# Optimization experiments

Measured on AMD Instinct MI355X. Metric: run time of the kernel, lower is better.

The kernel has to match this reference:

```python
import jax, jax.numpy as jnp
import numpy as np

N_NODES = 100000
N_EDGES = 200000
N_ATOM_FEATS = 56
HIDDEN = 256
N_GRAPHS = 2048
OUT_DIM = 1
EPS = 1e-5  # torch BatchNorm1d default


def setup_inputs() -> dict:
    key = jax.random.key(0)
    ks = jax.random.split(key, 10)
    x = jax.random.randint(ks[0], (N_NODES, N_ATOM_FEATS), 0, 2, dtype=jnp.int64 if jax.config.jax_enable_x64 else jnp.int32)
    edge_index = jax.random.randint(ks[1], (2, N_EDGES), 0, N_NODES)
    batch = jnp.sort(jax.random.randint(ks[2], (N_NODES,), 0, N_GRAPHS))
    emb_tables = jax.random.normal(ks[3], (N_ATOM_FEATS, 2, HIDDEN), dtype=jnp.float32) * 0.1
    Ws = jax.random.normal(ks[4], (3, HIDDEN, HIDDEN), dtype=jnp.float32) * (1.0 / np.sqrt(HIDDEN))
    bs = jnp.zeros((3, HIDDEN), dtype=jnp.float32)
    gammas = jnp.ones((2, HIDDEN), dtype=jnp.float32)
    betas = jnp.zeros((2, HIDDEN), dtype=jnp.float32)
    lin_w = jax.random.normal(ks[5], (HIDDEN, OUT_DIM), dtype=jnp.float32) * (1.0 / np.sqrt(HIDDEN))
    lin_b = jnp.zeros((OUT_DIM,), dtype=jnp.float32)
    return {"x": x, "edge_index": edge_index, "batch": batch, "emb_tables": emb_tables,
            "Ws": Ws, "bs": bs, "gammas": gammas, "betas": betas, "lin_w": lin_w, "lin_b": lin_b}


def reference(x, edge_index, batch, emb_tables, Ws, bs, gammas, betas, lin_w, lin_b):
    n = x.shape[0]
    # --- AtomEncoder: sum of 56 per-feature embedding lookups ---
    # emb_tables: [56, 2, H]; x: [N, 56] -> gathered [N, 56, H] -> sum over feature axis
    feat_idx = jnp.arange(x.shape[1])[None, :]  # [1,56]
    h = emb_tables[feat_idx, x].sum(axis=1)      # [N, H]

    # --- GCN normalization with self-loops (shared across layers) ---
    loops = jnp.arange(n)
    src = jnp.concatenate([edge_index[0], loops])
    dst = jnp.concatenate([edge_index[1], loops])
    deg = jax.ops.segment_sum(jnp.ones_like(src, dtype=h.dtype), dst, num_segments=n)
    dinv = jnp.where(deg > 0, jax.lax.rsqrt(deg), 0.0)
    norm = dinv[src] * dinv[dst]  # [E+N]

    def gcn_conv(h, W, b):
        hw = h @ W                                   # [N, H']
        msg = hw[src] * norm[:, None]                # gather + scale
        agg = jax.ops.segment_sum(msg, dst, num_segments=n)  # scatter-add
        return agg + b

    # --- layers 0..L-2: conv -> batchnorm (batch stats) -> relu; eval => no dropout ---
    for i in range(2):
        h = gcn_conv(h, Ws[i], bs[i])
        mu = h.mean(axis=0)
        var = h.var(axis=0)
        h = (h - mu) * jax.lax.rsqrt(var + EPS) * gammas[i] + betas[i]
        h = jax.nn.relu(h)
    # --- last conv (return_embeds=True: no softmax) ---
    h = gcn_conv(h, Ws[2], bs[2])

    # --- global mean pool over graphs ---
    sums = jax.ops.segment_sum(h, batch, num_segments=N_GRAPHS)          # [G, H]
    counts = jax.ops.segment_sum(jnp.ones((n,), h.dtype), batch, num_segments=N_GRAPHS)
    pooled = sums / jnp.maximum(counts, 1.0)[:, None]

    return pooled @ lin_w + lin_b  # [G, OUT_DIM]
```

## Files before the change

### kernel.cpp

```cpp
#include <hip/hip_runtime.h>
#include <hip/hip_bf16.h>

#define NN 100000
#define NE 200000
#define NF 56
#define HD 256
#define NG 2048

#define SCAN_CH 512
#define NCH ((NN + SCAN_CH - 1) / SCAN_CH)
#define EB ((NE + 255) / 256)

#define PB 2048
#define AB 2048
#define ZB 98

typedef __bf16 bf16x8 __attribute__((ext_vector_type(8)));
typedef __bf16 bf16x4 __attribute__((ext_vector_type(4)));
typedef float  floatx4 __attribute__((ext_vector_type(4)));

__global__ void prep_params(const float* __restrict__ emb, const float* __restrict__ Ws,
                            const float* __restrict__ bs, const float* __restrict__ lw,
                            __bf16* __restrict__ dW0t, float* __restrict__ bW0,
                            float* __restrict__ w2lw, float* __restrict__ b2lw,
                            __bf16* __restrict__ Wt, unsigned* __restrict__ deg) {
    __shared__ float row[HD];
    int c = threadIdx.x;
    int f = blockIdx.x;
    if (f >= NF + 2) {
        int g = f - (NF + 2);
        if (g < HD) {
            Wt[(size_t)g * HD + c] = (__bf16)Ws[(size_t)HD * HD + (size_t)c * HD + g];
        } else {
            int idx = (g - HD) * HD + c;
            if (idx < NN / 4) ((int4*)deg)[idx] = make_int4(0, 0, 0, 0);
        }
        return;
    }
    if (f == NF + 1) {
        const float* W2 = Ws + (size_t)2 * HD * HD;
        float acc = 0.f;
        for (int k = 0; k < HD; ++k) acc += W2[(size_t)c * HD + k] * lw[k];
        w2lw[c] = acc;
        row[c] = bs[2 * HD + c] * lw[c];
        __syncthreads();
        for (int off = 128; off > 0; off >>= 1) {
            if (c < off) row[c] += row[c + off];
            __syncthreads();
        }
        if (c == 0) *b2lw = row[0];
        return;
    }
    if (f < NF) {
        row[c] = emb[(f * 2 + 1) * HD + c] - emb[(f * 2 + 0) * HD + c];
    } else {
        float s = 0.f;
        for (int ff = 0; ff < NF; ++ff) s += emb[(ff * 2) * HD + c];
        row[c] = s;
    }
    __syncthreads();
    float acc = 0.f;
    for (int k = 0; k < HD; ++k) acc += row[k] * Ws[k * HD + c];
    if (f < NF) {
        dW0t[c * 64 + f] = (__bf16)acc;
    } else {
        bW0[c] = acc;
        #pragma unroll
        for (int k = NF; k < 64; ++k) dW0t[c * 64 + k] = (__bf16)0.f;
    }
}

__global__ void deg_kernel(const int* __restrict__ dst, unsigned* __restrict__ deg, int E) {
    int e = blockIdx.x * blockDim.x + threadIdx.x;
    if (e < E) atomicAdd(&deg[dst[e]], 1u);
}

__global__ void chunk_sum_dinv(const unsigned* __restrict__ deg, unsigned* __restrict__ csum,
                               float* __restrict__ dinv, float* __restrict__ selfn) {
    __shared__ unsigned s[SCAN_CH];
    int t = threadIdx.x;
    int base = blockIdx.x * SCAN_CH;
    unsigned v = (base + t < NN) ? deg[base + t] : 0u;
    s[t] = v;
    if (base + t < NN) {
        float d = (float)(v + 1u);
        dinv[base + t]  = rsqrtf(d);
        selfn[base + t] = 1.0f / d;
    }
    __syncthreads();
    for (int off = SCAN_CH / 2; off > 0; off >>= 1) {
        if (t < off) s[t] += s[t + off];
        __syncthreads();
    }
    if (t == 0) csum[blockIdx.x] = s[0];
}

__global__ void chunk_apply(const unsigned* __restrict__ deg, const unsigned* __restrict__ csum,
                            unsigned* __restrict__ row_start, unsigned* __restrict__ cursor) {
    __shared__ unsigned s[SCAN_CH];
    __shared__ unsigned cs[256];
    int t = threadIdx.x;
    if (t < 256) cs[t] = (t < NCH) ? csum[t] : 0u;
    __syncthreads();
    for (int off = 1; off < 256; off <<= 1) {
        unsigned add = (t < 256 && t >= off) ? cs[t - off] : 0u;
        __syncthreads();
        if (t < 256) cs[t] += add;
        __syncthreads();
    }
    unsigned chunk_base = (blockIdx.x == 0) ? 0u : cs[blockIdx.x - 1];

    int base = blockIdx.x * SCAN_CH;
    unsigned v = (base + t < NN) ? deg[base + t] : 0u;
    s[t] = v;
    __syncthreads();
    for (int off = 1; off < SCAN_CH; off <<= 1) {
        unsigned add = (t >= off) ? s[t - off] : 0u;
        __syncthreads();
        s[t] += add;
        __syncthreads();
    }
    if (base + t < NN) {
        unsigned rs = chunk_base + s[t] - v;
        row_start[base + t] = rs;
        cursor[base + t] = rs;
    }
    if (blockIdx.x == 0 && t == 0) row_start[NN] = NE;
}

__global__ void csr_fill_gb(const int* __restrict__ src, const int* __restrict__ dst,
                            const float* __restrict__ dinv, unsigned* __restrict__ cursor,
                            int* __restrict__ ecol, float* __restrict__ enorm,
                            const int* __restrict__ batch, unsigned* __restrict__ gstart) {
    int t = threadIdx.x;
    if (blockIdx.x < EB) {
        int e = blockIdx.x * 256 + t;
        if (e < NE) {
            int s = src[e], d = dst[e];
            unsigned pos = atomicAdd(&cursor[d], 1u);
            ecol[pos] = s;
            enorm[pos] = dinv[s] * dinv[d];
        }
    } else {
        int g = (blockIdx.x - EB) * 256 + t;
        if (g <= NG) {
            int lo = 0, hi = NN;
            while (lo < hi) {
                int mid = (lo + hi) >> 1;
                if (batch[mid] < g) lo = mid + 1; else hi = mid;
            }
            gstart[g] = (unsigned)lo;
        }
    }
}

#define ELSTR 68
__global__ void __launch_bounds__(512) encoder_mfma(const int* __restrict__ x,
                                                    const __bf16* __restrict__ dW0t,
                                                    const float* __restrict__ bW0,
                                                    __bf16* __restrict__ C) {
    __shared__ __bf16 sA[128 * ELSTR];
    __shared__ __bf16 sB[256 * ELSTR];
    int t = threadIdx.x;
    int m0 = blockIdx.x * 128;
    int lane = t & 63, w = t >> 6;
    int quad = lane >> 4, l16 = lane & 15;
    int mw = (w & 1) * 64, nw = (w >> 1) * 64;

    {
        int r = t >> 2;
        int kh = (t & 3) * 16;
        int row = m0 + r;
        int nreal = (kh < 48) ? 16 : 8;
        #pragma unroll
        for (int j = 0; j < 4; ++j) {
            bf16x4 b;
            if (row < NN && j * 4 < nreal) {
                int4 iv = *(const int4*)&x[(size_t)row * NF + kh + j * 4];
                b[0] = (__bf16)(float)iv.x;
                b[1] = (__bf16)(float)iv.y;
                b[2] = (__bf16)(float)iv.z;
                b[3] = (__bf16)(float)iv.w;
            } else {
                b[0] = b[1] = b[2] = b[3] = (__bf16)0.f;
            }
            *(bf16x4*)&sA[r * ELSTR + kh + j * 4] = b;
        }
    }
    {
        int bn = t >> 1;
        int kh = (t & 1) * 32;
        #pragma unroll
        for (int j = 0; j < 4; ++j) {
            bf16x8 v = *(const bf16x8*)&dW0t[(size_t)bn * 64 + kh + j * 8];
            *(bf16x8*)&sB[bn * ELSTR + kh + j * 8] = v;
        }
    }
    __syncthreads();

    floatx4 acc[4][4] = {};
    #pragma unroll
    for (int s = 0; s < 2; ++s) {
        bf16x8 af[4], bfr[4];
        #pragma unroll
        for (int i = 0; i < 4; ++i)
            af[i] = *(const bf16x8*)&sA[(mw + i * 16 + l16) * ELSTR + s * 32 + quad * 8];
        #pragma unroll
        for (int i = 0; i < 4; ++i)
            bfr[i] = *(const bf16x8*)&sB[(nw + i * 16 + l16) * ELSTR + s * 32 + quad * 8];
        #pragma unroll
        for (int mi = 0; mi < 4; ++mi)
            #pragma unroll
            for (int ni = 0; ni < 4; ++ni)
                acc[mi][ni] = __builtin_amdgcn_mfma_f32_16x16x32_bf16(
                    af[mi], bfr[ni], acc[mi][ni], 0, 0, 0);
    }

    float bw[4];
    #pragma unroll
    for (int ni = 0; ni < 4; ++ni) bw[ni] = bW0[nw + ni * 16 + l16];
    #pragma unroll
    for (int mi = 0; mi < 4; ++mi) {
        #pragma unroll
        for (int r = 0; r < 4; ++r) {
            int row = m0 + mw + mi * 16 + quad * 4 + r;
            if (row < NN) {
                #pragma unroll
                for (int ni = 0; ni < 4; ++ni)
                    C[(size_t)row * HD + nw + ni * 16 + l16] =
                        (__bf16)(acc[mi][ni][r] + bw[ni]);
            }
        }
    }
}

#define LSTR 36
__global__ void __launch_bounds__(512) gemm_mfma(const __bf16* __restrict__ A,
                                                 const __bf16* __restrict__ Wt,
                                                 __bf16* __restrict__ C, int M,
                                                 const float* __restrict__ ascale,
                                                 const float* __restrict__ ashift) {
    __shared__ __bf16 sA[128 * LSTR];
    __shared__ __bf16 sB[256 * LSTR];
    int t = threadIdx.x;
    int m0 = blockIdx.x * 128;
    int lane = t & 63, w = t >> 6;
    int quad = lane >> 4, l16 = lane & 15;
    int mw = (w & 1) * 64;
    int nw = (w >> 1) * 64;

    int ar = t >> 2;
    int ak = (t & 3) * 8;
    int bn = t >> 1;
    int bk = (t & 1) * 16;

    auto ldA = [&](int k0, bf16x8& pa) {
        float4 s0 = *(const float4*)&ascale[k0 + ak];
        float4 s1 = *(const float4*)&ascale[k0 + ak + 4];
        float4 h0 = *(const float4*)&ashift[k0 + ak];
        float4 h1 = *(const float4*)&ashift[k0 + ak + 4];
        int row = m0 + ar;
        bf16x8 a = {};
        if (row < M) a = *(const bf16x8*)&A[(size_t)row * HD + k0 + ak];
        bf16x8 b;
        b[0] = (__bf16)fmaxf((float)a[0] * s0.x + h0.x, 0.f);
        b[1] = (__bf16)fmaxf((float)a[1] * s0.y + h0.y, 0.f);
        b[2] = (__bf16)fmaxf((float)a[2] * s0.z + h0.z, 0.f);
        b[3] = (__bf16)fmaxf((float)a[3] * s0.w + h0.w, 0.f);
        b[4] = (__bf16)fmaxf((float)a[4] * s1.x + h1.x, 0.f);
        b[5] = (__bf16)fmaxf((float)a[5] * s1.y + h1.y, 0.f);
        b[6] = (__bf16)fmaxf((float)a[6] * s1.z + h1.z, 0.f);
        b[7] = (__bf16)fmaxf((float)a[7] * s1.w + h1.w, 0.f);
        pa = b;
    };
    auto ldB = [&](int k0, bf16x8 pb[2]) {
        #pragma unroll
        for (int j = 0; j < 2; ++j)
            pb[j] = *(const bf16x8*)&Wt[(size_t)bn * HD + k0 + bk + j * 8];
    };

    bf16x8 pa, pb[2];
    ldA(0, pa);
    ldB(0, pb);

    floatx4 acc[4][4] = {};

    for (int k0 = 0; k0 < 256; k0 += 32) {
        *(bf16x8*)&sA[ar * LSTR + ak] = pa;
        *(bf16x8*)&sB[bn * LSTR + bk]     = pb[0];
        *(bf16x8*)&sB[bn * LSTR + bk + 8] = pb[1];
        __syncthreads();

        if (k0 + 32 < 256) {
            ldA(k0 + 32, pa);
            ldB(k0 + 32, pb);
        }

        bf16x8 af[4], bfr[4];
        #pragma unroll
        for (int i = 0; i < 4; ++i)
            af[i] = *(const bf16x8*)&sA[(mw + i * 16 + l16) * LSTR + quad * 8];
        #pragma unroll
        for (int i = 0; i < 4; ++i)
            bfr[i] = *(const bf16x8*)&sB[(nw + i * 16 + l16) * LSTR + quad * 8];
        #pragma unroll
        for (int mi = 0; mi < 4; ++mi)
            #pragma unroll
            for (int ni = 0; ni < 4; ++ni)
                acc[mi][ni] = __builtin_amdgcn_mfma_f32_16x16x32_bf16(
                    af[mi], bfr[ni], acc[mi][ni], 0, 0, 0);
        __syncthreads();
    }

    #pragma unroll
    for (int mi = 0; mi < 4; ++mi) {
        #pragma unroll
        for (int r = 0; r < 4; ++r) {
            int row = m0 + mw + mi * 16 + quad * 4 + r;
            if (row < M) {
                #pragma unroll
                for (int ni = 0; ni < 4; ++ni)
                    C[(size_t)row * HD + nw + ni * 16 + l16] = (__bf16)acc[mi][ni][r];
            }
        }
    }
}

__global__ void __launch_bounds__(256) gcn_aggregate(const __bf16* __restrict__ hw,
                                                     const float* __restrict__ selfn,
                                                     const float* __restrict__ bias,
                                                     const unsigned* __restrict__ row_start,
                                                     const int* __restrict__ ecol,
                                                     const float* __restrict__ enorm,
                                                     __bf16* __restrict__ agg,
                                                     float* __restrict__ part) {
    int t = threadIdx.x;
    int l = t & 63, w = t >> 6;
    int c4 = l * 4;
    float4 bv = *(const float4*)&bias[c4];
    float4 lsum = make_float4(0.f, 0.f, 0.f, 0.f);
    float4 lssq = make_float4(0.f, 0.f, 0.f, 0.f);

    for (int n = blockIdx.x * 4 + w; n < NN; n += AB * 4) {
        float s = selfn[n];
        bf16x4 hv = *(const bf16x4*)&hw[(size_t)n * HD + c4];
        float4 acc;
        acc.x = (float)hv[0] * s + bv.x;
        acc.y = (float)hv[1] * s + bv.y;
        acc.z = (float)hv[2] * s + bv.z;
        acc.w = (float)hv[3] * s + bv.w;
        unsigned e0 = row_start[n], e1 = row_start[n + 1];
        unsigned e = e0;
        for (; e + 4 <= e1; e += 4) {
            int sv0 = ecol[e], sv1 = ecol[e + 1], sv2 = ecol[e + 2], sv3 = ecol[e + 3];
            float nm0 = enorm[e], nm1 = enorm[e + 1], nm2 = enorm[e + 2], nm3 = enorm[e + 3];
            bf16x4 u0 = *(const bf16x4*)&hw[(size_t)sv0 * HD + c4];
            bf16x4 u1 = *(const bf16x4*)&hw[(size_t)sv1 * HD + c4];
            bf16x4 u2 = *(const bf16x4*)&hw[(size_t)sv2 * HD + c4];
            bf16x4 u3 = *(const bf16x4*)&hw[(size_t)sv3 * HD + c4];
            acc.x += (float)u0[0] * nm0 + (float)u1[0] * nm1 + (float)u2[0] * nm2 + (float)u3[0] * nm3;
            acc.y += (float)u0[1] * nm0 + (float)u1[1] * nm1 + (float)u2[1] * nm2 + (float)u3[1] * nm3;
            acc.z += (float)u0[2] * nm0 + (float)u1[2] * nm1 + (float)u2[2] * nm2 + (float)u3[2] * nm3;
            acc.w += (float)u0[3] * nm0 + (float)u1[3] * nm1 + (float)u2[3] * nm2 + (float)u3[3] * nm3;
        }
        for (; e + 2 <= e1; e += 2) {
            int sv0 = ecol[e], sv1 = ecol[e + 1];
            float nm0 = enorm[e], nm1 = enorm[e + 1];
            bf16x4 u0 = *(const bf16x4*)&hw[(size_t)sv0 * HD + c4];
            bf16x4 u1 = *(const bf16x4*)&hw[(size_t)sv1 * HD + c4];
            acc.x += (float)u0[0] * nm0 + (float)u1[0] * nm1;
            acc.y += (float)u0[1] * nm0 + (float)u1[1] * nm1;
            acc.z += (float)u0[2] * nm0 + (float)u1[2] * nm1;
            acc.w += (float)u0[3] * nm0 + (float)u1[3] * nm1;
        }
        if (e < e1) {
            int sv = ecol[e];
            float nm = enorm[e];
            bf16x4 u = *(const bf16x4*)&hw[(size_t)sv * HD + c4];
            acc.x += (float)u[0] * nm;
            acc.y += (float)u[1] * nm;
            acc.z += (float)u[2] * nm;
            acc.w += (float)u[3] * nm;
        }
        bf16x4 o;
        o[0] = (__bf16)acc.x; o[1] = (__bf16)acc.y;
        o[2] = (__bf16)acc.z; o[3] = (__bf16)acc.w;
        *(bf16x4*)&agg[(size_t)n * HD + c4] = o;

        lsum.x += acc.x; lsum.y += acc.y; lsum.z += acc.z; lsum.w += acc.w;
        lssq.x += acc.x * acc.x; lssq.y += acc.y * acc.y;
        lssq.z += acc.z * acc.z; lssq.w += acc.w * acc.w;
    }

    __shared__ float4 ssum[4][64];
    __shared__ float4 sss[4][64];
    ssum[w][l] = lsum;
    sss[w][l]  = lssq;
    __syncthreads();
    if (w == 0) {
        float4 a0 = ssum[0][l], a1 = ssum[1][l], a2 = ssum[2][l], a3 = ssum[3][l];
        float4 q0 = sss[0][l],  q1 = sss[1][l],  q2 = sss[2][l],  q3 = sss[3][l];
        part[(c4 + 0) * AB + blockIdx.x] = a0.x + a1.x + a2.x + a3.x;
        part[(c4 + 1) * AB + blockIdx.x] = a0.y + a1.y + a2.y + a3.y;
        part[(c4 + 2) * AB + blockIdx.x] = a0.z + a1.z + a2.z + a3.z;
        part[(c4 + 3) * AB + blockIdx.x] = a0.w + a1.w + a2.w + a3.w;
        part[(HD + c4 + 0) * AB + blockIdx.x] = q0.x + q1.x + q2.x + q3.x;
        part[(HD + c4 + 1) * AB + blockIdx.x] = q0.y + q1.y + q2.y + q3.y;
        part[(HD + c4 + 2) * AB + blockIdx.x] = q0.z + q1.z + q2.z + q3.z;
        part[(HD + c4 + 3) * AB + blockIdx.x] = q0.w + q1.w + q2.w + q3.w;
    }
}

__global__ void __launch_bounds__(256) bn_scale(const float* __restrict__ part,
                                                const float* __restrict__ gamma,
                                                const float* __restrict__ beta,
                                                float* __restrict__ scale,
                                                float* __restrict__ shift) {
    __shared__ float rs[256], rq[256];
    int t = threadIdx.x;
    int c = blockIdx.x;
    float s = 0.f, q = 0.f;
    for (int j = t; j < PB; j += 256) {
        s += part[c * PB + j];
        q += part[(HD + c) * PB + j];
    }
    rs[t] = s; rq[t] = q;
    __syncthreads();
    for (int off = 128; off > 0; off >>= 1) {
        if (t < off) { rs[t] += rs[t + off]; rq[t] += rq[t + off]; }
        __syncthreads();
    }
    if (t == 0) {
        const float inv_n = 1.0f / (float)NN;
        float mu  = rs[0] * inv_n;
        float var = rq[0] * inv_n - mu * mu;
        float rstd = rsqrtf(var + 1e-5f);
        float sc = gamma[c] * rstd;
        scale[c] = sc;
        shift[c] = beta[c] - mu * sc;
    }
}

__global__ void __launch_bounds__(256) bn_dot(const __bf16* __restrict__ h,
                                              const float* __restrict__ scale,
                                              const float* __restrict__ shift,
                                              const float* __restrict__ w2lw,
                                              float* __restrict__ z) {
    int tid = blockIdx.x * 256 + threadIdx.x;
    int n = tid >> 6;
    if (n >= NN) return;
    int l = tid & 63;
    int c4 = l * 4;
    bf16x4 a = *(const bf16x4*)&h[(size_t)n * HD + c4];
    float4 sc = *(const float4*)&scale[c4];
    float4 sh = *(const float4*)&shift[c4];
    float4 wv = *(const float4*)&w2lw[c4];
    float d = fmaxf((float)a[0] * sc.x + sh.x, 0.f) * wv.x
            + fmaxf((float)a[1] * sc.y + sh.y, 0.f) * wv.y
            + fmaxf((float)a[2] * sc.z + sh.z, 0.f) * wv.z
            + fmaxf((float)a[3] * sc.w + sh.w, 0.f) * wv.w;
    #pragma unroll
    for (int off = 32; off > 0; off >>= 1) d += __shfl_down(d, off, 64);
    if (l == 0) z[n] = d;
}

__global__ void __launch_bounds__(256) pool_fused(const float* __restrict__ z,
                                                  const float* __restrict__ selfn,
                                                  const float* __restrict__ b2lw,
                                                  const unsigned* __restrict__ row_start,
                                                  const int* __restrict__ ecol,
                                                  const float* __restrict__ enorm,
                                                  const unsigned* __restrict__ gstart,
                                                  const float* __restrict__ lb,
                                                  float* __restrict__ out) {
    int tid = blockIdx.x * 256 + threadIdx.x;
    int g = tid >> 6;
    if (g >= NG) return;
    int l = tid & 63;
    unsigned s0 = gstart[g], s1 = gstart[g + 1];
    float bb = *b2lw;
    float s = 0.f;
    for (unsigned i = s0 + l; i < s1; i += 64) {
        float d = selfn[i] * z[i] + bb;
        unsigned e0 = row_start[i], e1 = row_start[i + 1];
        for (unsigned e = e0; e < e1; ++e)
            d += enorm[e] * z[ecol[e]];
        s += d;
    }
    #pragma unroll
    for (int off = 32; off > 0; off >>= 1) s += __shfl_down(s, off, 64);
    if (l == 0) out[g] = s / fmaxf((float)(s1 - s0), 1.0f) + lb[0];
}

extern "C" void kernel_launch(void* const* d_in, const int* in_sizes, int n_in,
                              void* d_out, int out_size, void* d_ws, size_t ws_size,
                              hipStream_t stream) {
    const int*   x     = (const int*)d_in[0];
    const int*   ei    = (const int*)d_in[1];
    const int*   batch = (const int*)d_in[2];
    const float* emb   = (const float*)d_in[3];
    const float* Ws    = (const float*)d_in[4];
    const float* bs    = (const float*)d_in[5];
    const float* gam   = (const float*)d_in[6];
    const float* bet   = (const float*)d_in[7];
    const float* lw    = (const float*)d_in[8];
    const float* lb    = (const float*)d_in[9];
    float* out = (float*)d_out;

    const int* src = ei;
    const int* dst = ei + NE;

    char* p = (char*)d_ws;
    size_t off = 0;
    auto carve = [&](size_t bytes) { void* r = p + off; off = (off + bytes + 255) & ~(size_t)255; return r; };
    __bf16*   buf0   = (__bf16*)carve((size_t)NN * HD * 2);
    __bf16*   buf1   = (__bf16*)carve((size_t)NN * HD * 2);
    float*    bW0    = (float*)carve(HD * 4);
    __bf16*   dW0t   = (__bf16*)carve(HD * 64 * 2);
    __bf16*   Wt     = (__bf16*)carve((size_t)HD * HD * 2);
    float*    w2lw   = (float*)carve(HD * 4);
    float*    b2lw   = (float*)carve(256);
    unsigned* deg    = (unsigned*)carve(NN * 4);
    float*    dinv   = (float*)carve(NN * 4);
    float*    selfn  = (float*)carve(NN * 4);
    unsigned* csum   = (unsigned*)carve(256 * 4);
    unsigned* row_s  = (unsigned*)carve((NN + 1) * 4);
    unsigned* cursor = (unsigned*)carve(NN * 4);
    int*      ecol   = (int*)carve(NE * 4);
    float*    enorm  = (float*)carve(NE * 4);
    float*    part   = (float*)carve((size_t)2 * HD * PB * 4);
    float*    scale  = (float*)carve(HD * 4);
    float*    shift  = (float*)carve(HD * 4);
    unsigned* gstart = (unsigned*)carve((NG + 1) * 4);
    float*    zbuf   = (float*)carve(NN * 4);
    (void)ws_size; (void)n_in; (void)in_sizes; (void)out_size;

    prep_params<<<NF + 2 + HD + ZB, HD, 0, stream>>>(
        emb, Ws, bs, lw, dW0t, bW0, w2lw, b2lw, Wt, deg);

    deg_kernel<<<(NE + 255) / 256, 256, 0, stream>>>(dst, deg, NE);
    chunk_sum_dinv<<<NCH, SCAN_CH, 0, stream>>>(deg, csum, dinv, selfn);
    chunk_apply<<<NCH, SCAN_CH, 0, stream>>>(deg, csum, row_s, cursor);
    csr_fill_gb<<<EB + (NG + 256) / 256, 256, 0, stream>>>(
        src, dst, dinv, cursor, ecol, enorm, batch, gstart);

    encoder_mfma<<<(NN + 127) / 128, 512, 0, stream>>>(x, dW0t, bW0, buf1);
    gcn_aggregate<<<AB, 256, 0, stream>>>(
        buf1, selfn, bs, row_s, ecol, enorm, buf0, part);
    bn_scale<<<HD, 256, 0, stream>>>(part, gam, bet, scale, shift);

    gemm_mfma<<<(NN + 127) / 128, 512, 0, stream>>>(
        buf0, Wt, buf1, NN, scale, shift);
    gcn_aggregate<<<AB, 256, 0, stream>>>(
        buf1, selfn, bs + HD, row_s, ecol, enorm, buf0, part);
    bn_scale<<<HD, 256, 0, stream>>>(part, gam + HD, bet + HD, scale, shift);

    bn_dot<<<(NN * 64 + 255) / 256, 256, 0, stream>>>(buf0, scale, shift, w2lw, zbuf);
    pool_fused<<<(NG * 64 + 255) / 256, 256, 0, stream>>>(
        zbuf, selfn, b2lw, row_s, ecol, enorm, gstart, lb, out);
}
```

Baseline: 290.1 us.

## Aggregate 64-wide encoder inputs before first GEMM instead of 256-wide features

Uses linearity of the first GCN layer: the binary atom features (plus a constant-1 column carrying the embedding base term) are aggregated over the graph in a 64-wide bf16 space, then multiplied by the folded embedding-times-W0 matrix. This replaces the first 256-wide gather/scatter aggregation pass with a much narrower one. The encoder GEMM now also emits the BatchNorm partial sums, and the partial-sum layout becomes row-major per block so bn_scale takes a variable block count. Extra costs are an x-to-bf16 conversion pass and bf16 rounding of the aggregated inputs before the GEMM.

New measurement: 274.1 us. 5.5% less time.

```diff
diff --git a/kernel.cpp b/kernel.cpp
--- a/kernel.cpp
+++ b/kernel.cpp
@@ -11,9 +11,10 @@
 #define NCH ((NN + SCAN_CH - 1) / SCAN_CH)
 #define EB ((NE + 255) / 256)
 
-#define PB 2048
 #define AB 2048
 #define ZB 98
+#define CVB ((NN + 255) / 256)
+#define ENB ((NN + 127) / 128)
 
 typedef __bf16 bf16x8 __attribute__((ext_vector_type(8)));
 typedef __bf16 bf16x4 __attribute__((ext_vector_type(4)));
@@ -21,9 +22,10 @@
 
 __global__ void prep_params(const float* __restrict__ emb, const float* __restrict__ Ws,
                             const float* __restrict__ bs, const float* __restrict__ lw,
-                            __bf16* __restrict__ dW0t, float* __restrict__ bW0,
+                            __bf16* __restrict__ dW0t,
                             float* __restrict__ w2lw, float* __restrict__ b2lw,
-                            __bf16* __restrict__ Wt, unsigned* __restrict__ deg) {
+                            __bf16* __restrict__ Wt, unsigned* __restrict__ deg,
+                            const int* __restrict__ x, __bf16* __restrict__ xb) {
     __shared__ float row[HD];
     int c = threadIdx.x;
     int f = blockIdx.x;
@@ -31,9 +33,29 @@
         int g = f - (NF + 2);
         if (g < HD) {
             Wt[(size_t)g * HD + c] = (__bf16)Ws[(size_t)HD * HD + (size_t)c * HD + g];
-        } else {
+        } else if (g < HD + ZB) {
             int idx = (g - HD) * HD + c;
             if (idx < NN / 4) ((int4*)deg)[idx] = make_int4(0, 0, 0, 0);
+        } else {
+            int r = (g - HD - ZB) * 256 + c;
+            if (r < NN) {
+                const int* xr = x + (size_t)r * NF;
+                __bf16 o[64];
+                #pragma unroll
+                for (int j = 0; j < 14; ++j) {
+                    int4 iv = *(const int4*)&xr[j * 4];
+                    o[j * 4 + 0] = (__bf16)(float)iv.x;
+                    o[j * 4 + 1] = (__bf16)(float)iv.y;
+                    o[j * 4 + 2] = (__bf16)(float)iv.z;
+                    o[j * 4 + 3] = (__bf16)(float)iv.w;
+                }
+                o[56] = (__bf16)1.0f;
+                #pragma unroll
+                for (int j = 57; j < 64; ++j) o[j] = (__bf16)0.0f;
+                #pragma unroll
+                for (int j = 0; j < 8; ++j)
+                    *(bf16x8*)&xb[(size_t)r * 64 + j * 8] = *(const bf16x8*)&o[j * 8];
+            }
         }
         return;
     }
@@ -64,9 +86,9 @@
     if (f < NF) {
         dW0t[c * 64 + f] = (__bf16)acc;
     } else {
-        bW0[c] = acc;
-        #pragma unroll
-        for (int k = NF; k < 64; ++k) dW0t[c * 64 + k] = (__bf16)0.f;
+        dW0t[c * 64 + 56] = (__bf16)acc;
+        #pragma unroll
+        for (int k = 57; k < 64; ++k) dW0t[c * 64 + k] = (__bf16)0.f;
     }
 }
 
@@ -154,13 +176,41 @@
     }
 }
 
+__global__ void __launch_bounds__(256) agg_x(const __bf16* __restrict__ xb,
+                                             const float* __restrict__ selfn,
+                                             const unsigned* __restrict__ row_start,
+                                             const int* __restrict__ ecol,
+                                             const float* __restrict__ enorm,
+                                             __bf16* __restrict__ ax) {
+    int tid = blockIdx.x * 256 + threadIdx.x;
+    int n = tid >> 6;
+    if (n >= NN) return;
+    int l = tid & 63;
+    float acc = (float)xb[(size_t)n * 64 + l] * selfn[n];
+    unsigned e0 = row_start[n], e1 = row_start[n + 1];
+    unsigned e = e0;
+    for (; e + 2 <= e1; e += 2) {
+        int s0 = ecol[e], s1 = ecol[e + 1];
+        float n0 = enorm[e], n1 = enorm[e + 1];
+        float v0 = (float)xb[(size_t)s0 * 64 + l];
+        float v1 = (float)xb[(size_t)s1 * 64 + l];
+        acc += v0 * n0 + v1 * n1;
+    }
+    if (e < e1)
+        acc += (float)xb[(size_t)ecol[e] * 64 + l] * enorm[e];
+    ax[(size_t)n * 64 + l] = (__bf16)acc;
+}
+
 #define ELSTR 68
-__global__ void __launch_bounds__(512) encoder_mfma(const int* __restrict__ x,
-                                                    const __bf16* __restrict__ dW0t,
-                                                    const float* __restrict__ bW0,
-                                                    __bf16* __restrict__ C) {
+__global__ void __launch_bounds__(512) enc_gemm(const __bf16* __restrict__ ax,
+                                                const __bf16* __restrict__ dW0t,
+                                                const float* __restrict__ b0,
+                                                __bf16* __restrict__ C,
+                                                float* __restrict__ part) {
     __shared__ __bf16 sA[128 * ELSTR];
     __shared__ __bf16 sB[256 * ELSTR];
+    __shared__ float psum[8][64];
+    __shared__ float psq[8][64];
     int t = threadIdx.x;
     int m0 = blockIdx.x * 128;
     int lane = t & 63, w = t >> 6;
@@ -169,32 +219,23 @@
 
     {
         int r = t >> 2;
-        int kh = (t & 3) * 16;
+        int k = (t & 3) * 16;
         int row = m0 + r;
-        int nreal = (kh < 48) ? 16 : 8;
-        #pragma unroll
-        for (int j = 0; j < 4; ++j) {
-            bf16x4 b;
-            if (row < NN && j * 4 < nreal) {
-                int4 iv = *(const int4*)&x[(size_t)row * NF + kh + j * 4];
-                b[0] = (__bf16)(float)iv.x;
-                b[1] = (__bf16)(float)iv.y;
-                b[2] = (__bf16)(float)iv.z;
-                b[3] = (__bf16)(float)iv.w;
-            } else {
-                b[0] = b[1] = b[2] = b[3] = (__bf16)0.f;
-            }
-            *(bf16x4*)&sA[r * ELSTR + kh + j * 4] = b;
-        }
+        bf16x8 v0 = {}, v1 = {};
+        if (row < NN) {
+            v0 = *(const bf16x8*)&ax[(size_t)row * 64 + k];
+            v1 = *(const bf16x8*)&ax[(size_t)row * 64 + k + 8];
+        }
+        *(bf16x8*)&sA[r * ELSTR + k]     = v0;
+        *(bf16x8*)&sA[r * ELSTR + k + 8] = v1;
     }
     {
         int bn = t >> 1;
         int kh = (t & 1) * 32;
         #pragma unroll
-        for (int j = 0; j < 4; ++j) {
-            bf16x8 v = *(const bf16x8*)&dW0t[(size_t)bn * 64 + kh + j * 8];
-            *(bf16x8*)&sB[bn * ELSTR + kh + j * 8] = v;
-        }
+        for (int j = 0; j < 4; ++j)
+            *(bf16x8*)&sB[bn * ELSTR + kh + j * 8] =
+                *(const bf16x8*)&dW0t[(size_t)bn * 64 + kh + j * 8];
     }
     __syncthreads();
 
@@ -218,7 +259,9 @@
 
     float bw[4];
     #pragma unroll
-    for (int ni = 0; ni < 4; ++ni) bw[ni] = bW0[nw + ni * 16 + l16];
+    for (int ni = 0; ni < 4; ++ni) bw[ni] = b0[nw + ni * 16 + l16];
+    float ls[4] = {0.f, 0.f, 0.f, 0.f};
+    float lq[4] = {0.f, 0.f, 0.f, 0.f};
     #pragma unroll
     for (int mi = 0; mi < 4; ++mi) {
         #pragma unroll
@@ -226,10 +269,36 @@
             int row = m0 + mw + mi * 16 + quad * 4 + r;
             if (row < NN) {
                 #pragma unroll
-                for (int ni = 0; ni < 4; ++ni)
-                    C[(size_t)row * HD + nw + ni * 16 + l16] =
-                        (__bf16)(acc[mi][ni][r] + bw[ni]);
+                for (int ni = 0; ni < 4; ++ni) {
+                    float v = acc[mi][ni][r] + bw[ni];
+                    C[(size_t)row * HD + nw + ni * 16 + l16] = (__bf16)v;
+                    ls[ni] += v;
+                    lq[ni] += v * v;
+                }
             }
+        }
+    }
+    #pragma unroll
+    for (int ni = 0; ni < 4; ++ni) {
+        ls[ni] += __shfl_xor(ls[ni], 16, 64);
+        ls[ni] += __shfl_xor(ls[ni], 32, 64);
+        lq[ni] += __shfl_xor(lq[ni], 16, 64);
+        lq[ni] += __shfl_xor(lq[ni], 32, 64);
+    }
+    if (lane < 16) {
+        #pragma unroll
+        for (int ni = 0; ni < 4; ++ni) {
+            psum[w][ni * 16 + l16] = ls[ni];
+            psq[w][ni * 16 + l16]  = lq[ni];
+        }
+    }
+    __syncthreads();
+    if (!(w & 1) && lane < 16) {
+        #pragma unroll
+        for (int ni = 0; ni < 4; ++ni) {
+            int ci = ni * 16 + l16;
+            part[(size_t)blockIdx.x * 512 + nw + ci]       = psum[w][ci] + psum[w + 1][ci];
+            part[(size_t)blockIdx.x * 512 + 256 + nw + ci] = psq[w][ci]  + psq[w + 1][ci];
         }
     }
 }
@@ -400,18 +469,21 @@
     if (w == 0) {
         float4 a0 = ssum[0][l], a1 = ssum[1][l], a2 = ssum[2][l], a3 = ssum[3][l];
         float4 q0 = sss[0][l],  q1 = sss[1][l],  q2 = sss[2][l],  q3 = sss[3][l];
-        part[(c4 + 0) * AB + blockIdx.x] = a0.x + a1.x + a2.x + a3.x;
-        part[(c4 + 1) * AB + blockIdx.x] = a0.y + a1.y + a2.y + a3.y;
-        part[(c4 + 2) * AB + blockIdx.x] = a0.z + a1.z + a2.z + a3.z;
-        part[(c4 + 3) * AB + blockIdx.x] = a0.w + a1.w + a2.w + a3.w;
-        part[(HD + c4 + 0) * AB + blockIdx.x] = q0.x + q1.x + q2.x + q3.x;
-        part[(HD + c4 + 1) * AB + blockIdx.x] = q0.y + q1.y + q2.y + q3.y;
-        part[(HD + c4 + 2) * AB + blockIdx.x] = q0.z + q1.z + q2.z + q3.z;
-        part[(HD + c4 + 3) * AB + blockIdx.x] = q0.w + q1.w + q2.w + q3.w;
-    }
-}
-
-__global__ void __launch_bounds__(256) bn_scale(const float* __restrict__ part,
+        float4 sm, sq;
+        sm.x = a0.x + a1.x + a2.x + a3.x;
+        sm.y = a0.y + a1.y + a2.y + a3.y;
+        sm.z = a0.z + a1.z + a2.z + a3.z;
+        sm.w = a0.w + a1.w + a2.w + a3.w;
+        sq.x = q0.x + q1.x + q2.x + q3.x;
+        sq.y = q0.y + q1.y + q2.y + q3.y;
+        sq.z = q0.z + q1.z + q2.z + q3.z;
+        sq.w = q0.w + q1.w + q2.w + q3.w;
+        *(float4*)&part[(size_t)blockIdx.x * 512 + c4]       = sm;
+        *(float4*)&part[(size_t)blockIdx.x * 512 + 256 + c4] = sq;
+    }
+}
+
+__global__ void __launch_bounds__(256) bn_scale(const float* __restrict__ part, int nb,
                                                 const float* __restrict__ gamma,
                                                 const float* __restrict__ beta,
                                                 float* __restrict__ scale,
@@ -420,9 +492,9 @@
     int t = threadIdx.x;
     int c = blockIdx.x;
     float s = 0.f, q = 0.f;
-    for (int j = t; j < PB; j += 256) {
-        s += part[c * PB + j];
-        q += part[(HD + c) * PB + j];
+    for (int j = t; j < nb; j += 256) {
+        s += part[(size_t)j * 512 + c];
+        q += part[(size_t)j * 512 + 256 + c];
     }
     rs[t] = s; rq[t] = q;
     __syncthreads();
@@ -515,7 +587,8 @@
     auto carve = [&](size_t bytes) { void* r = p + off; off = (off + bytes + 255) & ~(size_t)255; return r; };
     __bf16*   buf0   = (__bf16*)carve((size_t)NN * HD * 2);
     __bf16*   buf1   = (__bf16*)carve((size_t)NN * HD * 2);
-    float*    bW0    = (float*)carve(HD * 4);
+    __bf16*   xb     = (__bf16*)carve((size_t)NN * 64 * 2);
+    __bf16*   ax     = (__bf16*)carve((size_t)NN * 64 * 2);
     __bf16*   dW0t   = (__bf16*)carve(HD * 64 * 2);
     __bf16*   Wt     = (__bf16*)carve((size_t)HD * HD * 2);
     float*    w2lw   = (float*)carve(HD * 4);
@@ -528,15 +601,15 @@
     unsigned* cursor = (unsigned*)carve(NN * 4);
     int*      ecol   = (int*)carve(NE * 4);
     float*    enorm  = (float*)carve(NE * 4);
-    float*    part   = (float*)carve((size_t)2 * HD * PB * 4);
+    float*    part   = (float*)carve((size_t)AB * 512 * 4);
     float*    scale  = (float*)carve(HD * 4);
     float*    shift  = (float*)carve(HD * 4);
     unsigned* gstart = (unsigned*)carve((NG + 1) * 4);
     float*    zbuf   = (float*)carve(NN * 4);
     (void)ws_size; (void)n_in; (void)in_sizes; (void)out_size;
 
-    prep_params<<<NF + 2 + HD + ZB, HD, 0, stream>>>(
-        emb, Ws, bs, lw, dW0t, bW0, w2lw, b2lw, Wt, deg);
+    prep_params<<<NF + 2 + HD + ZB + CVB, HD, 0, stream>>>(
+        emb, Ws, bs, lw, dW0t, w2lw, b2lw, Wt, deg, x, xb);
 
     deg_kernel<<<(NE + 255) / 256, 256, 0, stream>>>(dst, deg, NE);
     chunk_sum_dinv<<<NCH, SCAN_CH, 0, stream>>>(deg, csum, dinv, selfn);
@@ -544,16 +617,15 @@
     csr_fill_gb<<<EB + (NG + 256) / 256, 256, 0, stream>>>(
         src, dst, dinv, cursor, ecol, enorm, batch, gstart);
 
-    encoder_mfma<<<(NN + 127) / 128, 512, 0, stream>>>(x, dW0t, bW0, buf1);
-    gcn_aggregate<<<AB, 256, 0, stream>>>(
-        buf1, selfn, bs, row_s, ecol, enorm, buf0, part);
-    bn_scale<<<HD, 256, 0, stream>>>(part, gam, bet, scale, shift);
-
-    gemm_mfma<<<(NN + 127) / 128, 512, 0, stream>>>(
-        buf0, Wt, buf1, NN, scale, shift);
+    agg_x<<<(NN * 64 + 255) / 256, 256, 0, stream>>>(
+        xb, selfn, row_s, ecol, enorm, ax);
+    enc_gemm<<<ENB, 512, 0, stream>>>(ax, dW0t, bs, buf0, part);
+    bn_scale<<<HD, 256, 0, stream>>>(part, ENB, gam, bet, scale, shift);
+
+    gemm_mfma<<<ENB, 512, 0, stream>>>(buf0, Wt, buf1, NN, scale, shift);
     gcn_aggregate<<<AB, 256, 0, stream>>>(
         buf1, selfn, bs + HD, row_s, ecol, enorm, buf0, part);
-    bn_scale<<<HD, 256, 0, stream>>>(part, gam + HD, bet + HD, scale, shift);
+    bn_scale<<<HD, 256, 0, stream>>>(part, AB, gam + HD, bet + HD, scale, shift);
 
     bn_dot<<<(NN * 64 + 255) / 256, 256, 0, stream>>>(buf0, scale, shift, w2lw, zbuf);
     pool_fused<<<(NG * 64 + 255) / 256, 256, 0, stream>>>(
```
